# Kernel tuning notes

Measured on AMD Instinct MI355X. Metric: run time of the kernel, lower is better.

Reference implementation:

```python
import jax, jax.numpy as jnp
import numpy as np

D_MODEL = 1024
N_HEADS = 16
HEAD_DIM = D_MODEL // N_HEADS


def setup_inputs() -> dict:
    key = jax.random.key(0)
    k_x, k_qkv, k_out = jax.random.split(key, 3)
    x = jax.random.normal(k_x, (4, 2048, D_MODEL), dtype=jnp.float32)
    # nn.Linear weights are (out_features, in_features); init std=0.02
    w_qkv = jax.random.normal(k_qkv, (3 * D_MODEL, D_MODEL), dtype=jnp.float32) * 0.02
    w_out = jax.random.normal(k_out, (D_MODEL, D_MODEL), dtype=jnp.float32) * 0.02
    return {"x": x, "w_qkv": w_qkv, "w_out": w_out}


def reference(x, w_qkv, w_out):
    B, T, C = x.shape
    H, Dh = N_HEADS, HEAD_DIM
    # qkv projection: x @ w_qkv.T -> (B, T, 3C)
    qkv = jnp.einsum('btc,oc->bto', x, w_qkv)
    q, k, v = jnp.split(qkv, 3, axis=-1)

    def split_heads(t):
        return t.reshape(B, T, H, Dh).transpose(0, 2, 1, 3)  # (B, H, T, Dh)

    q, k, v = split_heads(q), split_heads(k), split_heads(v)
    scale = jnp.sqrt(jnp.asarray(Dh, dtype=x.dtype))
    scores = jnp.einsum('bhqd,bhkd->bhqk', q, k) / scale  # (B, H, T, T)
    causal = jnp.tril(jnp.ones((T, T), dtype=bool))
    scores = jnp.where(causal[None, None], scores, jnp.asarray(-jnp.inf, dtype=scores.dtype))
    attn = jax.nn.softmax(scores, axis=-1)
    out = jnp.einsum('bhqk,bhkd->bhqd', attn, v)  # (B, H, T, Dh)
    out = out.transpose(0, 2, 1, 3).reshape(B, T, C)
    return jnp.einsum('btc,oc->bto', out, w_out)
```

## Files before the change

### kernel.cpp

```cpp
#include <hip/hip_runtime.h>

typedef __attribute__((ext_vector_type(8))) short bf16x8;
typedef __attribute__((ext_vector_type(4))) float f32x4;
typedef __attribute__((ext_vector_type(16))) float f32x16;
typedef __attribute__((ext_vector_type(4))) int i32x4;
using u16 = unsigned short;

constexpr int Bsz = 4, T = 2048, C = 1024, H = 16, Dh = 64;
constexpr int Mrows = Bsz * T;
constexpr int K_DIM = 1024;
constexpr float QSCALE = 0.18033688011112042f;

__device__ inline u16 f2bf(float f) {
    unsigned u = __builtin_bit_cast(unsigned, f);
    u += 0x7FFFu + ((u >> 16) & 1u);
    return (u16)(u >> 16);
}

__device__ inline void g2l16(const void* g, void* l) {
    __builtin_amdgcn_global_load_lds((const __attribute__((address_space(1))) void*)g,
                                     (__attribute__((address_space(3))) void*)l, 16, 0, 0);
}

__device__ inline unsigned pk2(float lo, float hi) {
    unsigned d;
    asm("v_cvt_pk_bf16_f32 %0, %1, %2" : "=v"(d) : "v"(lo), "v"(hi));
    return d;
}
__device__ inline void swap32(unsigned& a, unsigned& b) {
    asm("v_permlane32_swap_b32 %0, %1" : "+v"(a), "+v"(b));
}

__global__ __launch_bounds__(256)
void cvt_k(const float* __restrict__ x, const float* __restrict__ wq,
           const float* __restrict__ wo, u16* __restrict__ xb,
           u16* __restrict__ wqb, u16* __restrict__ wob)
{
    int idx = blockIdx.x * 256 + threadIdx.x;
    const float* src; u16* dst; int rel;
    if (idx < 1048576)      { src = x;  dst = xb;  rel = idx; }
    else if (idx < 1441792) { src = wq; dst = wqb; rel = idx - 1048576; }
    else                    { src = wo; dst = wob; rel = idx - 1441792; }
    size_t off = (size_t)rel * 8;
    float4 a = *(const float4*)(src + off);
    float4 b = *(const float4*)(src + off + 4);
    unsigned r0 = (unsigned)f2bf(a.x) | ((unsigned)f2bf(a.y) << 16);
    unsigned r1 = (unsigned)f2bf(a.z) | ((unsigned)f2bf(a.w) << 16);
    unsigned r2 = (unsigned)f2bf(b.x) | ((unsigned)f2bf(b.y) << 16);
    unsigned r3 = (unsigned)f2bf(b.z) | ((unsigned)f2bf(b.w) << 16);
    *(uint4*)(dst + off) = make_uint4(r0, r1, r2, r3);
}

__device__ inline void stage_g(u16* lds, const u16* gb, int ldg, int tid) {
    #pragma unroll
    for (int i = 0; i < 4; ++i) {
        int ch = i * 256 + tid;
        int r = ch >> 3, c8 = ch & 7;
        int sc = c8 ^ (r & 7);
        g2l16(gb + (size_t)r * ldg + sc * 8, lds + (i * 256 + (tid & 192)) * 8);
    }
}

template<int MODE>
__device__ __forceinline__
void gemm_body(const u16* __restrict__ Ab, const u16* __restrict__ Bb,
               float* __restrict__ Op, u16* __restrict__ qws,
               u16* __restrict__ kws, u16* __restrict__ vtws,
               u16* As, u16* Bs, int m0, int n0)
{
    const int tid = threadIdx.x;
    const int l = tid & 63, wid = tid >> 6;
    const int wm = wid >> 1, wn = wid & 1;
    const int lane16 = l & 15, lhi = l >> 4;

    const u16* Abase = Ab + (size_t)m0 * K_DIM;
    const u16* Bbase = Bb + (size_t)n0 * K_DIM;

    f32x4 acc[4][4] = {};

    for (int ks = 0; ks < K_DIM / 64; ++ks) {
        __syncthreads();
        stage_g(As, Abase + ks * 64, K_DIM, tid);
        stage_g(Bs, Bbase + ks * 64, K_DIM, tid);
        __syncthreads();
        #pragma unroll
        for (int kc = 0; kc < 2; kc++) {
            bf16x8 af[4], bfr[4];
            #pragma unroll
            for (int mi = 0; mi < 4; mi++) {
                int row = wm * 64 + mi * 16 + lane16;
                int byte = row * 128 + kc * 64 + lhi * 16; byte ^= (row & 7) << 4;
                af[mi] = *(const bf16x8*)((const char*)As + byte);
            }
            #pragma unroll
            for (int ni = 0; ni < 4; ni++) {
                int row = wn * 64 + ni * 16 + lane16;
                int byte = row * 128 + kc * 64 + lhi * 16; byte ^= (row & 7) << 4;
                bfr[ni] = *(const bf16x8*)((const char*)Bs + byte);
            }
            #pragma unroll
            for (int mi = 0; mi < 4; mi++)
                #pragma unroll
                for (int ni = 0; ni < 4; ni++) {
                    if constexpr (MODE == 2)
                        acc[mi][ni] = __builtin_amdgcn_mfma_f32_16x16x32_bf16(
                            bfr[ni], af[mi], acc[mi][ni], 0, 0, 0);
                    else
                        acc[mi][ni] = __builtin_amdgcn_mfma_f32_16x16x32_bf16(
                            af[mi], bfr[ni], acc[mi][ni], 0, 0, 0);
                }
        }
    }

    if constexpr (MODE == 2) {
        #pragma unroll
        for (int mi = 0; mi < 4; mi++)
            #pragma unroll
            for (int ni = 0; ni < 4; ni++)
                #pragma unroll
                for (int r = 0; r < 4; r++) {
                    int wr = n0 + wn * 64 + ni * 16 + lhi * 4 + r;
                    int tg = m0 + wm * 64 + mi * 16 + lane16;
                    int hh = (wr >> 6) & 15, d = wr & 63;
                    int bb = tg >> 11, tt = tg & 2047;
                    size_t off = (((size_t)bb * H + hh) * Dh + d) * T + tt;
                    vtws[off] = f2bf(acc[mi][ni][r]);
                }
    } else {
        #pragma unroll
        for (int mi = 0; mi < 4; mi++)
            #pragma unroll
            for (int ni = 0; ni < 4; ni++)
                #pragma unroll
                for (int r = 0; r < 4; r++) {
                    int gm = m0 + wm * 64 + mi * 16 + lhi * 4 + r;
                    int gn = n0 + wn * 64 + ni * 16 + lane16;
                    float val = acc[mi][ni][r];
                    if constexpr (MODE == 0) {
                        int hh = (gn >> 6) & 15, d = gn & 63;
                        int bb = gm >> 11, t = gm & 2047;
                        size_t off = (((size_t)bb * H + hh) * T + t) * Dh + d;
                        if (gn < C) qws[off] = f2bf(val * QSCALE);
                        else        kws[off] = f2bf(val);
                    } else {
                        Op[(size_t)gm * C + gn] = val;
                    }
                }
    }
}

__global__ __launch_bounds__(256)
void gemm_qkv(const u16* __restrict__ xb, const u16* __restrict__ wqkvb,
              u16* __restrict__ qws, u16* __restrict__ kws, u16* __restrict__ vtws)
{
    __shared__ alignas(16) u16 As[128 * 64];
    __shared__ alignas(16) u16 Bs[128 * 64];
    const int m0 = blockIdx.x * 128;
    if (blockIdx.y < 16)
        gemm_body<0>(xb, wqkvb, nullptr, qws, kws, vtws, As, Bs, m0, blockIdx.y * 128);
    else
        gemm_body<2>(xb, wqkvb, nullptr, qws, kws, vtws, As, Bs, m0,
                     2 * C + (blockIdx.y - 16) * 128);
}

__global__ __launch_bounds__(256)
void gemm_out(const u16* __restrict__ ob, const u16* __restrict__ woutb,
              float* __restrict__ Op)
{
    __shared__ alignas(16) u16 As[128 * 64];
    __shared__ alignas(16) u16 Bs[128 * 64];
    gemm_body<1>(ob, woutb, Op, nullptr, nullptr, nullptr, As, Bs,
                 blockIdx.x * 128, blockIdx.y * 128);
}

__device__ inline bf16x8 ldsfrag(const u16* base, int row, int cc) {
    int byte = (row << 7) + (cc << 4); byte ^= (row & 7) << 4;
    return *(const bf16x8*)((const char*)base + byte);
}

__device__ inline void stage_t(u16* lds, const u16* gb, int rstride, int tid) {
    #pragma unroll
    for (int it = 0; it < 2; ++it) {
        int chunk = it * 256 + tid;
        int r = chunk >> 3, cc = chunk & 7;
        int sc = cc ^ (r & 7);
        g2l16(gb + (size_t)r * rstride + sc * 8, lds + (it * 256 + (tid & 192)) * 8);
    }
}

__global__ __launch_bounds__(256, 3)
void attn_k(const u16* __restrict__ qws, const u16* __restrict__ kws,
            const u16* __restrict__ vtws, u16* __restrict__ ows)
{
    __shared__ alignas(16) u16 KL[3][64 * 64];
    __shared__ alignas(16) u16 VL[3][64 * 64];

    const int bid = blockIdx.x;
    const int head = bid & 63;
    const int qt = 15 - (bid >> 6);
    const int b = head >> 4, h = head & 15;
    const int tid = threadIdx.x, w = tid >> 6, l = tid & 63;
    const int l31 = l & 31, hi = l >> 5;

    const size_t hoff = (size_t)head * (T * Dh);
    const u16* Qg  = qws + hoff;
    const u16* Kg  = kws + hoff;
    const u16* Vtg = vtws + hoff;

    const int qb = qt * 128;
    const int nt = 2 * qt + 2;
    const int qbw = qb + w * 32;

    bf16x8 qf[4];
    #pragma unroll
    for (int c = 0; c < 4; ++c)
        qf[c] = *(const bf16x8*)(Qg + (size_t)(qbw + l31) * Dh + c * 16 + hi * 8);

    f32x16 o0{}, o1{};
    float mrun = -__builtin_inff(), lrun = 0.f;

    stage_t(KL[0], Kg, Dh, tid);
    stage_t(VL[0], Vtg, T, tid);
    stage_t(KL[1], Kg + (size_t)64 * Dh, Dh, tid);
    stage_t(VL[1], Vtg + 64, T, tid);

    int cur = 0;
    for (int t = 0; t < nt; ++t) {
        if (t + 1 < nt) asm volatile("s_waitcnt vmcnt(4)" ::: "memory");
        else            asm volatile("s_waitcnt vmcnt(0)" ::: "memory");
        __builtin_amdgcn_s_barrier();
        __builtin_amdgcn_sched_barrier(0);

        int nx = cur + 2; if (nx >= 3) nx -= 3;
        if (t + 2 < nt) {
            stage_t(KL[nx], Kg + (size_t)(t + 2) * 64 * Dh, Dh, tid);
            stage_t(VL[nx], Vtg + (t + 2) * 64, T, tid);
        }

        const int kv0 = t * 64;
        if (kv0 <= qbw + 31) {
            const u16* Kb = KL[cur];
            const u16* Vb = VL[cur];

            bf16x8 kf0[4], kf1[4];
            #pragma unroll
            for (int c = 0; c < 4; ++c) {
                kf0[c] = ldsfrag(Kb, l31, c * 2 + hi);
                kf1[c] = ldsfrag(Kb, 32 + l31, c * 2 + hi);
            }

            f32x16 s0{}, s1{};
            #pragma unroll
            for (int c = 0; c < 4; ++c) {
                s0 = __builtin_amdgcn_mfma_f32_32x32x16_bf16(kf0[c], qf[c], s0, 0, 0, 0);
                s1 = __builtin_amdgcn_mfma_f32_32x32x16_bf16(kf1[c], qf[c], s1, 0, 0, 0);
            }

            if (kv0 + 63 > qbw) {
                int qg = qbw + l31;
                #pragma unroll
                for (int r = 0; r < 16; ++r) {
                    int kvg = kv0 + (r & 3) + 8 * (r >> 2) + 4 * hi;
                    if (kvg > qg)      s0[r] = -__builtin_inff();
                    if (kvg + 32 > qg) s1[r] = -__builtin_inff();
                }
            }

            float m16[16];
            #pragma unroll
            for (int r = 0; r < 16; ++r) m16[r] = fmaxf(s0[r], s1[r]);
            #pragma unroll
            for (int d = 8; d; d >>= 1)
                #pragma unroll
                for (int r = 0; r < d; ++r) m16[r] = fmaxf(m16[r], m16[r + d]);
            float pmax = fmaxf(m16[0], __shfl_xor(m16[0], 32));

            if (!__all(pmax - mrun <= 8.0f)) {
                float mn = fmaxf(mrun, pmax);
                float corr = __builtin_amdgcn_exp2f(mrun - mn);
                mrun = mn;
                lrun *= corr;
                #pragma unroll
                for (int r = 0; r < 16; ++r) {
                    float cr = __shfl(corr, (r & 3) + 8 * (r >> 2) + 4 * hi);
                    o0[r] *= cr;
                    o1[r] *= cr;
                }
            }
            float p0[16], p1[16];
            float t0 = 0.f, t1 = 0.f, t2 = 0.f, t3 = 0.f;
            #pragma unroll
            for (int r = 0; r < 16; ++r) {
                p0[r] = __builtin_amdgcn_exp2f(s0[r] - mrun);
                p1[r] = __builtin_amdgcn_exp2f(s1[r] - mrun);
                float s = p0[r] + p1[r];
                if ((r & 3) == 0) t0 += s; else if ((r & 3) == 1) t1 += s;
                else if ((r & 3) == 2) t2 += s; else t3 += s;
            }
            lrun += (t0 + t1) + (t2 + t3);

            unsigned paf[4][4];
            unsigned cc[8];
            #pragma unroll
            for (int i = 0; i < 4; ++i) cc[i]     = pk2(p0[2 * i], p0[2 * i + 1]);
            #pragma unroll
            for (int i = 0; i < 4; ++i) cc[4 + i] = pk2(p0[8 + 2 * i], p0[9 + 2 * i]);
            swap32(cc[0], cc[2]); swap32(cc[1], cc[3]);
            swap32(cc[4], cc[6]); swap32(cc[5], cc[7]);
            #pragma unroll
            for (int i = 0; i < 4; ++i) { paf[0][i] = cc[i]; paf[1][i] = cc[4 + i]; }
            #pragma unroll
            for (int i = 0; i < 4; ++i) cc[i]     = pk2(p1[2 * i], p1[2 * i + 1]);
            #pragma unroll
            for (int i = 0; i < 4; ++i) cc[4 + i] = pk2(p1[8 + 2 * i], p1[9 + 2 * i]);
            swap32(cc[0], cc[2]); swap32(cc[1], cc[3]);
            swap32(cc[4], cc[6]); swap32(cc[5], cc[7]);
            #pragma unroll
            for (int i = 0; i < 4; ++i) { paf[2][i] = cc[i]; paf[3][i] = cc[4 + i]; }

            #pragma unroll
            for (int kb = 0; kb < 4; ++kb) {
                i32x4 wv = {(int)paf[kb][0], (int)paf[kb][1],
                            (int)paf[kb][2], (int)paf[kb][3]};
                bf16x8 pa = __builtin_bit_cast(bf16x8, wv);
                bf16x8 v0 = ldsfrag(Vb, l31,      kb * 2 + hi);
                bf16x8 v1 = ldsfrag(Vb, 32 + l31, kb * 2 + hi);
                o0 = __builtin_amdgcn_mfma_f32_32x32x16_bf16(pa, v0, o0, 0, 0, 0);
                o1 = __builtin_amdgcn_mfma_f32_32x32x16_bf16(pa, v1, o1, 0, 0, 0);
            }
        }
        cur = (cur == 2) ? 0 : cur + 1;
    }

    float lt = lrun + __shfl_xor(lrun, 32);
    float inv = 1.0f / lt;
    #pragma unroll
    for (int r = 0; r < 16; ++r) {
        int cr = (r & 3) + 8 * (r >> 2) + 4 * hi;
        float il = __shfl(inv, cr);
        size_t rowoff = ((size_t)b * T + qb + w * 32 + cr) * C + h * Dh + l31;
        ows[rowoff]      = f2bf(o0[r] * il);
        ows[rowoff + 32] = f2bf(o1[r] * il);
    }
}

extern "C" void kernel_launch(void* const* d_in, const int* in_sizes, int n_in,
                              void* d_out, int out_size, void* d_ws, size_t ws_size,
                              hipStream_t stream)
{
    const float* x     = (const float*)d_in[0];
    const float* w_qkv = (const float*)d_in[1];
    const float* w_out = (const float*)d_in[2];
    float* out = (float*)d_out;

    const size_t SZ = (size_t)Bsz * H * T * Dh;
    u16* qws   = (u16*)d_ws;
    u16* kws   = qws + SZ;
    u16* vtws  = kws + SZ;
    u16* xb    = vtws + SZ;
    u16* ows   = xb;
    u16* wqkvb = xb + SZ;
    u16* woutb = wqkvb + (size_t)3 * C * C;

    cvt_k<<<dim3(6144), 256, 0, stream>>>(x, w_qkv, w_out, xb, wqkvb, woutb);

    gemm_qkv<<<dim3(Mrows / 128, 24), 256, 0, stream>>>(xb, wqkvb, qws, kws, vtws);

    attn_k<<<dim3(1024), 256, 0, stream>>>(qws, kws, vtws, ows);

    gemm_out<<<dim3(Mrows / 128, C / 128), 256, 0, stream>>>(ows, woutb, out);
}
```

Baseline: 157.8 us.

## Replace GEMMs with 256-row tiles and a 4-stage async LDS pipeline

Rewrites the QKV and output-projection GEMMs as a templated 512-thread kernel with 256-row M tiles and a 4-buffer LDS ring over K=32 slices. Loads are issued three stages ahead and waited on with explicit vmcnt counts instead of two block-wide syncs per step. The QKV projection is split into two launches: Q/K with BN=256 and V-transpose with BN=128. The aim is to overlap global loads with MFMA work and raise data reuse per tile. In exchange it uses more LDS and registers per block, and each launch has only 256 blocks.

```diff
diff --git a/kernel.cpp b/kernel.cpp
--- a/kernel.cpp
+++ b/kernel.cpp
@@ -29,6 +29,14 @@
 }
 __device__ inline void swap32(unsigned& a, unsigned& b) {
     asm("v_permlane32_swap_b32 %0, %1" : "+v"(a), "+v"(b));
+}
+
+template<int N> __device__ inline void waitv() {
+    if constexpr (N == 0)      asm volatile("s_waitcnt vmcnt(0)" ::: "memory");
+    else if constexpr (N == 3) asm volatile("s_waitcnt vmcnt(3)" ::: "memory");
+    else if constexpr (N == 4) asm volatile("s_waitcnt vmcnt(4)" ::: "memory");
+    else if constexpr (N == 6) asm volatile("s_waitcnt vmcnt(6)" ::: "memory");
+    else if constexpr (N == 8) asm volatile("s_waitcnt vmcnt(8)" ::: "memory");
 }
 
 __global__ __launch_bounds__(256)
@@ -51,76 +59,97 @@
     *(uint4*)(dst + off) = make_uint4(r0, r1, r2, r3);
 }
 
-__device__ inline void stage_g(u16* lds, const u16* gb, int ldg, int tid) {
+template<int ROWS>
+__device__ inline void stage_q(u16* lds, const u16* gb, int tid) {
     #pragma unroll
-    for (int i = 0; i < 4; ++i) {
-        int ch = i * 256 + tid;
-        int r = ch >> 3, c8 = ch & 7;
-        int sc = c8 ^ (r & 7);
-        g2l16(gb + (size_t)r * ldg + sc * 8, lds + (i * 256 + (tid & 192)) * 8);
-    }
-}
-
-template<int MODE>
-__device__ __forceinline__
-void gemm_body(const u16* __restrict__ Ab, const u16* __restrict__ Bb,
-               float* __restrict__ Op, u16* __restrict__ qws,
-               u16* __restrict__ kws, u16* __restrict__ vtws,
-               u16* As, u16* Bs, int m0, int n0)
+    for (int i = 0; i < ROWS / 128; ++i) {
+        int ch = i * 512 + tid;
+        int r = ch >> 2, c4 = ch & 3;
+        int sc = c4 ^ ((r >> 1) & 3);
+        g2l16(gb + (size_t)r * K_DIM + sc * 8, lds + (i * 512 + (tid & 448)) * 8);
+    }
+}
+
+__device__ inline bf16x8 ldsfragq(const u16* base, int row, int lhi) {
+    int byte = (row << 6) + (lhi << 4); byte ^= ((row >> 1) & 3) << 4;
+    return *(const bf16x8*)((const char*)base + byte);
+}
+
+template<int MODE, int BN>
+__global__ __launch_bounds__(512, 2)
+void g256(const u16* __restrict__ Ab, const u16* __restrict__ Bb,
+          float* __restrict__ Op, u16* __restrict__ qws,
+          u16* __restrict__ kws, u16* __restrict__ vtws)
 {
+    constexpr int NWN = BN / 64;
+    constexpr int WM  = 8 / NWN;
+    constexpr int MI  = 256 / WM / 16;
+    constexpr int LPT = 2 + BN / 128;
+    constexpr int nK  = K_DIM / 32;
+
+    __shared__ alignas(16) u16 As[4][256 * 32];
+    __shared__ alignas(16) u16 Bs[4][BN * 32];
+
     const int tid = threadIdx.x;
     const int l = tid & 63, wid = tid >> 6;
-    const int wm = wid >> 1, wn = wid & 1;
+    const int wm = wid / NWN, wn = wid % NWN;
     const int lane16 = l & 15, lhi = l >> 4;
+    const int m0 = blockIdx.x * 256;
+    const int n0 = (MODE == 2 ? 2 * C : 0) + blockIdx.y * BN;
+    const int wrow0 = wm * (MI * 16);
 
     const u16* Abase = Ab + (size_t)m0 * K_DIM;
     const u16* Bbase = Bb + (size_t)n0 * K_DIM;
 
-    f32x4 acc[4][4] = {};
-
-    for (int ks = 0; ks < K_DIM / 64; ++ks) {
-        __syncthreads();
-        stage_g(As, Abase + ks * 64, K_DIM, tid);
-        stage_g(Bs, Bbase + ks * 64, K_DIM, tid);
-        __syncthreads();
-        #pragma unroll
-        for (int kc = 0; kc < 2; kc++) {
-            bf16x8 af[4], bfr[4];
-            #pragma unroll
-            for (int mi = 0; mi < 4; mi++) {
-                int row = wm * 64 + mi * 16 + lane16;
-                int byte = row * 128 + kc * 64 + lhi * 16; byte ^= (row & 7) << 4;
-                af[mi] = *(const bf16x8*)((const char*)As + byte);
-            }
-            #pragma unroll
-            for (int ni = 0; ni < 4; ni++) {
-                int row = wn * 64 + ni * 16 + lane16;
-                int byte = row * 128 + kc * 64 + lhi * 16; byte ^= (row & 7) << 4;
-                bfr[ni] = *(const bf16x8*)((const char*)Bs + byte);
-            }
-            #pragma unroll
-            for (int mi = 0; mi < 4; mi++)
-                #pragma unroll
-                for (int ni = 0; ni < 4; ni++) {
-                    if constexpr (MODE == 2)
-                        acc[mi][ni] = __builtin_amdgcn_mfma_f32_16x16x32_bf16(
-                            bfr[ni], af[mi], acc[mi][ni], 0, 0, 0);
-                    else
-                        acc[mi][ni] = __builtin_amdgcn_mfma_f32_16x16x32_bf16(
-                            af[mi], bfr[ni], acc[mi][ni], 0, 0, 0);
-                }
+    f32x4 acc[MI][4] = {};
+
+    stage_q<256>(As[0], Abase,      tid); stage_q<BN>(Bs[0], Bbase,      tid);
+    stage_q<256>(As[1], Abase + 32, tid); stage_q<BN>(Bs[1], Bbase + 32, tid);
+    stage_q<256>(As[2], Abase + 64, tid); stage_q<BN>(Bs[2], Bbase + 64, tid);
+
+    for (int t = 0; t < nK; ++t) {
+        const int cur = t & 3;
+        if (t + 2 < nK)      waitv<2 * LPT>();
+        else if (t + 1 < nK) waitv<LPT>();
+        else                 waitv<0>();
+        __builtin_amdgcn_s_barrier();
+        __builtin_amdgcn_sched_barrier(0);
+
+        if (t + 3 < nK) {
+            stage_q<256>(As[(t + 3) & 3], Abase + (t + 3) * 32, tid);
+            stage_q<BN> (Bs[(t + 3) & 3], Bbase + (t + 3) * 32, tid);
         }
+
+        bf16x8 bfr[4], af[MI];
+        #pragma unroll
+        for (int ni = 0; ni < 4; ++ni)
+            bfr[ni] = ldsfragq(Bs[cur], wn * 64 + ni * 16 + lane16, lhi);
+        #pragma unroll
+        for (int mi = 0; mi < MI; ++mi)
+            af[mi] = ldsfragq(As[cur], wrow0 + mi * 16 + lane16, lhi);
+
+        #pragma unroll
+        for (int mi = 0; mi < MI; ++mi)
+            #pragma unroll
+            for (int ni = 0; ni < 4; ++ni) {
+                if constexpr (MODE == 2)
+                    acc[mi][ni] = __builtin_amdgcn_mfma_f32_16x16x32_bf16(
+                        bfr[ni], af[mi], acc[mi][ni], 0, 0, 0);
+                else
+                    acc[mi][ni] = __builtin_amdgcn_mfma_f32_16x16x32_bf16(
+                        af[mi], bfr[ni], acc[mi][ni], 0, 0, 0);
+            }
     }
 
     if constexpr (MODE == 2) {
         #pragma unroll
-        for (int mi = 0; mi < 4; mi++)
+        for (int mi = 0; mi < MI; mi++)
             #pragma unroll
             for (int ni = 0; ni < 4; ni++)
                 #pragma unroll
                 for (int r = 0; r < 4; r++) {
                     int wr = n0 + wn * 64 + ni * 16 + lhi * 4 + r;
-                    int tg = m0 + wm * 64 + mi * 16 + lane16;
+                    int tg = m0 + wrow0 + mi * 16 + lane16;
                     int hh = (wr >> 6) & 15, d = wr & 63;
                     int bb = tg >> 11, tt = tg & 2047;
                     size_t off = (((size_t)bb * H + hh) * Dh + d) * T + tt;
@@ -128,12 +157,12 @@
                 }
     } else {
         #pragma unroll
-        for (int mi = 0; mi < 4; mi++)
+        for (int mi = 0; mi < MI; mi++)
             #pragma unroll
             for (int ni = 0; ni < 4; ni++)
                 #pragma unroll
                 for (int r = 0; r < 4; r++) {
-                    int gm = m0 + wm * 64 + mi * 16 + lhi * 4 + r;
+                    int gm = m0 + wrow0 + mi * 16 + lhi * 4 + r;
                     int gn = n0 + wn * 64 + ni * 16 + lane16;
                     float val = acc[mi][ni][r];
                     if constexpr (MODE == 0) {
@@ -149,30 +178,6 @@
     }
 }
 
-__global__ __launch_bounds__(256)
-void gemm_qkv(const u16* __restrict__ xb, const u16* __restrict__ wqkvb,
-              u16* __restrict__ qws, u16* __restrict__ kws, u16* __restrict__ vtws)
-{
-    __shared__ alignas(16) u16 As[128 * 64];
-    __shared__ alignas(16) u16 Bs[128 * 64];
-    const int m0 = blockIdx.x * 128;
-    if (blockIdx.y < 16)
-        gemm_body<0>(xb, wqkvb, nullptr, qws, kws, vtws, As, Bs, m0, blockIdx.y * 128);
-    else
-        gemm_body<2>(xb, wqkvb, nullptr, qws, kws, vtws, As, Bs, m0,
-                     2 * C + (blockIdx.y - 16) * 128);
-}
-
-__global__ __launch_bounds__(256)
-void gemm_out(const u16* __restrict__ ob, const u16* __restrict__ woutb,
-              float* __restrict__ Op)
-{
-    __shared__ alignas(16) u16 As[128 * 64];
-    __shared__ alignas(16) u16 Bs[128 * 64];
-    gemm_body<1>(ob, woutb, Op, nullptr, nullptr, nullptr, As, Bs,
-                 blockIdx.x * 128, blockIdx.y * 128);
-}
-
 __device__ inline bf16x8 ldsfrag(const u16* base, int row, int cc) {
     int byte = (row << 7) + (cc << 4); byte ^= (row & 7) << 4;
     return *(const bf16x8*)((const char*)base + byte);
@@ -364,9 +369,10 @@
 
     cvt_k<<<dim3(6144), 256, 0, stream>>>(x, w_qkv, w_out, xb, wqkvb, woutb);
 
-    gemm_qkv<<<dim3(Mrows / 128, 24), 256, 0, stream>>>(xb, wqkvb, qws, kws, vtws);
+    g256<0, 256><<<dim3(32, 8), 512, 0, stream>>>(xb, wqkvb, nullptr, qws, kws, vtws);
+    g256<2, 128><<<dim3(32, 8), 512, 0, stream>>>(xb, wqkvb, nullptr, qws, kws, vtws);
 
     attn_k<<<dim3(1024), 256, 0, stream>>>(qws, kws, vtws, ows);
 
-    gemm_out<<<dim3(Mrows / 128, C / 128), 256, 0, stream>>>(ows, woutb, out);
-}
+    g256<1, 128><<<dim3(32, 8), 512, 0, stream>>>(ows, woutb, out, nullptr, nullptr, nullptr);
+}
```

Measured after the change: 174.9 us. 10.9% more time.

## Use 2-wave attention blocks with 64 query rows per wave and reuse K/V fragments

Applied to the files above, without the earlier changes.

The attention kernel now runs 128 threads per block instead of 256. Each wave handles 64 query rows as two 32-row sub-tiles, and the K and V fragments it loads from LDS are shared by both sub-tiles. The LDS staging switches from an XOR-swizzled row layout to a column-chunk-major layout, so each fragment read is a contiguous 16-byte load. The aim is fewer LDS reads per MFMA. The cost is higher register pressure from two sets of accumulators and softmax state, fewer waves per block, a possible change in LDS bank conflicts, and more causal imbalance between the two sub-tiles.

```diff
diff --git a/kernel.cpp b/kernel.cpp
--- a/kernel.cpp
+++ b/kernel.cpp
@@ -173,22 +173,16 @@
                  blockIdx.x * 128, blockIdx.y * 128);
 }
 
-__device__ inline bf16x8 ldsfrag(const u16* base, int row, int cc) {
-    int byte = (row << 7) + (cc << 4); byte ^= (row & 7) << 4;
-    return *(const bf16x8*)((const char*)base + byte);
-}
-
-__device__ inline void stage_t(u16* lds, const u16* gb, int rstride, int tid) {
+__device__ inline void stage_c(u16* lds, const u16* gb, int rstride, int tid) {
     #pragma unroll
-    for (int it = 0; it < 2; ++it) {
-        int chunk = it * 256 + tid;
-        int r = chunk >> 3, cc = chunk & 7;
-        int sc = cc ^ (r & 7);
-        g2l16(gb + (size_t)r * rstride + sc * 8, lds + (it * 256 + (tid & 192)) * 8);
-    }
-}
-
-__global__ __launch_bounds__(256, 3)
+    for (int it = 0; it < 4; ++it) {
+        int i = it * 128 + tid;
+        int kv = i & 63, c8 = i >> 6;
+        g2l16(gb + (size_t)kv * rstride + c8 * 8, lds + i * 8);
+    }
+}
+
+__global__ __launch_bounds__(128, 2)
 void attn_k(const u16* __restrict__ qws, const u16* __restrict__ kws,
             const u16* __restrict__ vtws, u16* __restrict__ ows)
 {
@@ -209,138 +203,152 @@
 
     const int qb = qt * 128;
     const int nt = 2 * qt + 2;
-    const int qbw = qb + w * 32;
-
-    bf16x8 qf[4];
+    const int qbw = qb + w * 64;
+
+    bf16x8 qf[2][4];
     #pragma unroll
-    for (int c = 0; c < 4; ++c)
-        qf[c] = *(const bf16x8*)(Qg + (size_t)(qbw + l31) * Dh + c * 16 + hi * 8);
-
-    f32x16 o0{}, o1{};
-    float mrun = -__builtin_inff(), lrun = 0.f;
-
-    stage_t(KL[0], Kg, Dh, tid);
-    stage_t(VL[0], Vtg, T, tid);
-    stage_t(KL[1], Kg + (size_t)64 * Dh, Dh, tid);
-    stage_t(VL[1], Vtg + 64, T, tid);
+    for (int q2 = 0; q2 < 2; ++q2)
+        #pragma unroll
+        for (int c = 0; c < 4; ++c)
+            qf[q2][c] = *(const bf16x8*)(Qg + (size_t)(qbw + q2 * 32 + l31) * Dh
+                                         + c * 16 + hi * 8);
+
+    f32x16 oq[2][2] = {};
+    float mrun[2] = {-__builtin_inff(), -__builtin_inff()};
+    float lrun[2] = {0.f, 0.f};
+
+    stage_c(KL[0], Kg, Dh, tid);
+    stage_c(VL[0], Vtg, T, tid);
+    stage_c(KL[1], Kg + (size_t)64 * Dh, Dh, tid);
+    stage_c(VL[1], Vtg + 64, T, tid);
 
     int cur = 0;
     for (int t = 0; t < nt; ++t) {
-        if (t + 1 < nt) asm volatile("s_waitcnt vmcnt(4)" ::: "memory");
+        if (t + 1 < nt) asm volatile("s_waitcnt vmcnt(8)" ::: "memory");
         else            asm volatile("s_waitcnt vmcnt(0)" ::: "memory");
         __builtin_amdgcn_s_barrier();
         __builtin_amdgcn_sched_barrier(0);
 
         int nx = cur + 2; if (nx >= 3) nx -= 3;
         if (t + 2 < nt) {
-            stage_t(KL[nx], Kg + (size_t)(t + 2) * 64 * Dh, Dh, tid);
-            stage_t(VL[nx], Vtg + (t + 2) * 64, T, tid);
+            stage_c(KL[nx], Kg + (size_t)(t + 2) * 64 * Dh, Dh, tid);
+            stage_c(VL[nx], Vtg + (t + 2) * 64, T, tid);
         }
 
         const int kv0 = t * 64;
-        if (kv0 <= qbw + 31) {
-            const u16* Kb = KL[cur];
-            const u16* Vb = VL[cur];
-
-            bf16x8 kf0[4], kf1[4];
+        if (kv0 <= qbw + 63) {
+            const char* Kb = (const char*)KL[cur];
+            const char* Vb = (const char*)VL[cur];
+
+            bf16x8 kf0[4], kf1[4], vf0[4], vf1[4];
             #pragma unroll
             for (int c = 0; c < 4; ++c) {
-                kf0[c] = ldsfrag(Kb, l31, c * 2 + hi);
-                kf1[c] = ldsfrag(Kb, 32 + l31, c * 2 + hi);
+                int off = (c * 2 + hi) * 1024 + l31 * 16;
+                kf0[c] = *(const bf16x8*)(Kb + off);
+                kf1[c] = *(const bf16x8*)(Kb + off + 512);
+                vf0[c] = *(const bf16x8*)(Vb + off);
+                vf1[c] = *(const bf16x8*)(Vb + off + 512);
             }
 
-            f32x16 s0{}, s1{};
-            #pragma unroll
-            for (int c = 0; c < 4; ++c) {
-                s0 = __builtin_amdgcn_mfma_f32_32x32x16_bf16(kf0[c], qf[c], s0, 0, 0, 0);
-                s1 = __builtin_amdgcn_mfma_f32_32x32x16_bf16(kf1[c], qf[c], s1, 0, 0, 0);
-            }
-
-            if (kv0 + 63 > qbw) {
-                int qg = qbw + l31;
+            #pragma unroll
+            for (int q2 = 0; q2 < 2; ++q2) {
+                const int qbb = qbw + q2 * 32;
+                if (kv0 > qbb + 31) continue;
+
+                f32x16 s0{}, s1{};
+                #pragma unroll
+                for (int c = 0; c < 4; ++c) {
+                    s0 = __builtin_amdgcn_mfma_f32_32x32x16_bf16(kf0[c], qf[q2][c], s0, 0, 0, 0);
+                    s1 = __builtin_amdgcn_mfma_f32_32x32x16_bf16(kf1[c], qf[q2][c], s1, 0, 0, 0);
+                }
+
+                if (kv0 + 63 > qbb) {
+                    int qg = qbb + l31;
+                    #pragma unroll
+                    for (int r = 0; r < 16; ++r) {
+                        int kvg = kv0 + (r & 3) + 8 * (r >> 2) + 4 * hi;
+                        if (kvg > qg)      s0[r] = -__builtin_inff();
+                        if (kvg + 32 > qg) s1[r] = -__builtin_inff();
+                    }
+                }
+
+                float m16[16];
+                #pragma unroll
+                for (int r = 0; r < 16; ++r) m16[r] = fmaxf(s0[r], s1[r]);
+                #pragma unroll
+                for (int d = 8; d; d >>= 1)
+                    #pragma unroll
+                    for (int r = 0; r < d; ++r) m16[r] = fmaxf(m16[r], m16[r + d]);
+                float pmax = fmaxf(m16[0], __shfl_xor(m16[0], 32));
+
+                if (!__all(pmax - mrun[q2] <= 8.0f)) {
+                    float mn = fmaxf(mrun[q2], pmax);
+                    float corr = __builtin_amdgcn_exp2f(mrun[q2] - mn);
+                    mrun[q2] = mn;
+                    lrun[q2] *= corr;
+                    #pragma unroll
+                    for (int r = 0; r < 16; ++r) {
+                        float cr = __shfl(corr, (r & 3) + 8 * (r >> 2) + 4 * hi);
+                        oq[q2][0][r] *= cr;
+                        oq[q2][1][r] *= cr;
+                    }
+                }
+                float p0[16], p1[16];
+                float t0 = 0.f, t1 = 0.f, t2 = 0.f, t3 = 0.f;
                 #pragma unroll
                 for (int r = 0; r < 16; ++r) {
-                    int kvg = kv0 + (r & 3) + 8 * (r >> 2) + 4 * hi;
-                    if (kvg > qg)      s0[r] = -__builtin_inff();
-                    if (kvg + 32 > qg) s1[r] = -__builtin_inff();
-                }
-            }
-
-            float m16[16];
-            #pragma unroll
-            for (int r = 0; r < 16; ++r) m16[r] = fmaxf(s0[r], s1[r]);
-            #pragma unroll
-            for (int d = 8; d; d >>= 1)
-                #pragma unroll
-                for (int r = 0; r < d; ++r) m16[r] = fmaxf(m16[r], m16[r + d]);
-            float pmax = fmaxf(m16[0], __shfl_xor(m16[0], 32));
-
-            if (!__all(pmax - mrun <= 8.0f)) {
-                float mn = fmaxf(mrun, pmax);
-                float corr = __builtin_amdgcn_exp2f(mrun - mn);
-                mrun = mn;
-                lrun *= corr;
-                #pragma unroll
-                for (int r = 0; r < 16; ++r) {
-                    float cr = __shfl(corr, (r & 3) + 8 * (r >> 2) + 4 * hi);
-                    o0[r] *= cr;
-                    o1[r] *= cr;
-                }
-            }
-            float p0[16], p1[16];
-            float t0 = 0.f, t1 = 0.f, t2 = 0.f, t3 = 0.f;
-            #pragma unroll
-            for (int r = 0; r < 16; ++r) {
-                p0[r] = __builtin_amdgcn_exp2f(s0[r] - mrun);
-                p1[r] = __builtin_amdgcn_exp2f(s1[r] - mrun);
-                float s = p0[r] + p1[r];
-                if ((r & 3) == 0) t0 += s; else if ((r & 3) == 1) t1 += s;
-                else if ((r & 3) == 2) t2 += s; else t3 += s;
-            }
-            lrun += (t0 + t1) + (t2 + t3);
-
-            unsigned paf[4][4];
-            unsigned cc[8];
-            #pragma unroll
-            for (int i = 0; i < 4; ++i) cc[i]     = pk2(p0[2 * i], p0[2 * i + 1]);
-            #pragma unroll
-            for (int i = 0; i < 4; ++i) cc[4 + i] = pk2(p0[8 + 2 * i], p0[9 + 2 * i]);
-            swap32(cc[0], cc[2]); swap32(cc[1], cc[3]);
-            swap32(cc[4], cc[6]); swap32(cc[5], cc[7]);
-            #pragma unroll
-            for (int i = 0; i < 4; ++i) { paf[0][i] = cc[i]; paf[1][i] = cc[4 + i]; }
-            #pragma unroll
-            for (int i = 0; i < 4; ++i) cc[i]     = pk2(p1[2 * i], p1[2 * i + 1]);
-            #pragma unroll
-            for (int i = 0; i < 4; ++i) cc[4 + i] = pk2(p1[8 + 2 * i], p1[9 + 2 * i]);
-            swap32(cc[0], cc[2]); swap32(cc[1], cc[3]);
-            swap32(cc[4], cc[6]); swap32(cc[5], cc[7]);
-            #pragma unroll
-            for (int i = 0; i < 4; ++i) { paf[2][i] = cc[i]; paf[3][i] = cc[4 + i]; }
-
-            #pragma unroll
-            for (int kb = 0; kb < 4; ++kb) {
-                i32x4 wv = {(int)paf[kb][0], (int)paf[kb][1],
-                            (int)paf[kb][2], (int)paf[kb][3]};
-                bf16x8 pa = __builtin_bit_cast(bf16x8, wv);
-                bf16x8 v0 = ldsfrag(Vb, l31,      kb * 2 + hi);
-                bf16x8 v1 = ldsfrag(Vb, 32 + l31, kb * 2 + hi);
-                o0 = __builtin_amdgcn_mfma_f32_32x32x16_bf16(pa, v0, o0, 0, 0, 0);
-                o1 = __builtin_amdgcn_mfma_f32_32x32x16_bf16(pa, v1, o1, 0, 0, 0);
+                    p0[r] = __builtin_amdgcn_exp2f(s0[r] - mrun[q2]);
+                    p1[r] = __builtin_amdgcn_exp2f(s1[r] - mrun[q2]);
+                    float s = p0[r] + p1[r];
+                    if ((r & 3) == 0) t0 += s; else if ((r & 3) == 1) t1 += s;
+                    else if ((r & 3) == 2) t2 += s; else t3 += s;
+                }
+                lrun[q2] += (t0 + t1) + (t2 + t3);
+
+                unsigned paf[4][4];
+                unsigned cc[8];
+                #pragma unroll
+                for (int i = 0; i < 4; ++i) cc[i]     = pk2(p0[2 * i], p0[2 * i + 1]);
+                #pragma unroll
+                for (int i = 0; i < 4; ++i) cc[4 + i] = pk2(p0[8 + 2 * i], p0[9 + 2 * i]);
+                swap32(cc[0], cc[2]); swap32(cc[1], cc[3]);
+                swap32(cc[4], cc[6]); swap32(cc[5], cc[7]);
+                #pragma unroll
+                for (int i = 0; i < 4; ++i) { paf[0][i] = cc[i]; paf[1][i] = cc[4 + i]; }
+                #pragma unroll
+                for (int i = 0; i < 4; ++i) cc[i]     = pk2(p1[2 * i], p1[2 * i + 1]);
+                #pragma unroll
+                for (int i = 0; i < 4; ++i) cc[4 + i] = pk2(p1[8 + 2 * i], p1[9 + 2 * i]);
+                swap32(cc[0], cc[2]); swap32(cc[1], cc[3]);
+                swap32(cc[4], cc[6]); swap32(cc[5], cc[7]);
+                #pragma unroll
+                for (int i = 0; i < 4; ++i) { paf[2][i] = cc[i]; paf[3][i] = cc[4 + i]; }
+
+                #pragma unroll
+                for (int kb = 0; kb < 4; ++kb) {
+                    i32x4 wv = {(int)paf[kb][0], (int)paf[kb][1],
+                                (int)paf[kb][2], (int)paf[kb][3]};
+                    bf16x8 pa = __builtin_bit_cast(bf16x8, wv);
+                    oq[q2][0] = __builtin_amdgcn_mfma_f32_32x32x16_bf16(pa, vf0[kb], oq[q2][0], 0, 0, 0);
+                    oq[q2][1] = __builtin_amdgcn_mfma_f32_32x32x16_bf16(pa, vf1[kb], oq[q2][1], 0, 0, 0);
+                }
             }
         }
         cur = (cur == 2) ? 0 : cur + 1;
     }
 
-    float lt = lrun + __shfl_xor(lrun, 32);
-    float inv = 1.0f / lt;
     #pragma unroll
-    for (int r = 0; r < 16; ++r) {
-        int cr = (r & 3) + 8 * (r >> 2) + 4 * hi;
-        float il = __shfl(inv, cr);
-        size_t rowoff = ((size_t)b * T + qb + w * 32 + cr) * C + h * Dh + l31;
-        ows[rowoff]      = f2bf(o0[r] * il);
-        ows[rowoff + 32] = f2bf(o1[r] * il);
+    for (int q2 = 0; q2 < 2; ++q2) {
+        float lt = lrun[q2] + __shfl_xor(lrun[q2], 32);
+        float inv = 1.0f / lt;
+        #pragma unroll
+        for (int r = 0; r < 16; ++r) {
+            int cr = (r & 3) + 8 * (r >> 2) + 4 * hi;
+            float il = __shfl(inv, cr);
+            size_t rowoff = ((size_t)b * T + qbw + q2 * 32 + cr) * C + h * Dh + l31;
+            ows[rowoff]      = f2bf(oq[q2][0][r] * il);
+            ows[rowoff + 32] = f2bf(oq[q2][1][r] * il);
+        }
     }
 }
 
@@ -366,7 +374,7 @@
 
     gemm_qkv<<<dim3(Mrows / 128, 24), 256, 0, stream>>>(xb, wqkvb, qws, kws, vtws);
 
-    attn_k<<<dim3(1024), 256, 0, stream>>>(qws, kws, vtws, ows);
+    attn_k<<<dim3(1024), 128, 0, stream>>>(qws, kws, vtws, ows);
 
     gemm_out<<<dim3(Mrows / 128, C / 128), 256, 0, stream>>>(ows, woutb, out);
 }
```

New measurement: 183.3 us. +16.1%, slower.
